# Performance work log

Measured on AMD Instinct MI355X. Metric: run time of the kernel, lower is better.

Reference implementation:

```python
import jax, jax.numpy as jnp
import numpy as np

TEMPERATURE = 0.07
NUM_UNIFY_CLASSES = 256


def setup_inputs() -> dict:
    key = jax.random.key(0)
    k1, k2, k3 = jax.random.split(key, 3)
    b, c, h, w = 16, 256, 128, 128
    # small-magnitude feats so exp(logits) stays finite at temperature 0.07
    feats = jax.random.normal(k1, (b, c, h, w), dtype=jnp.float32) * 0.05
    queue = jax.random.normal(k2, (NUM_UNIFY_CLASSES, c), dtype=jnp.float32)
    queue = queue / jnp.linalg.norm(queue, axis=1, keepdims=True)  # unit rows, as a memory bank would hold
    labels = jax.random.randint(k3, (b * h * w, NUM_UNIFY_CLASSES), 0, 2, dtype=jnp.int32)
    return {"feats": feats, "queue": queue, "labels": labels}


def reference(feats, queue, labels):
    b, c, h, w = feats.shape
    # [b,c,h,w] -> [N, c]
    f = jnp.transpose(feats, (0, 2, 3, 1)).reshape(-1, c)
    # [N, M] logits
    logits = (f @ queue.T) / TEMPERATURE
    pos_mask = labels.reshape(-1, NUM_UNIFY_CLASSES).astype(logits.dtype)
    neg_mask = 1.0 - pos_mask
    sum_neg = jnp.sum(jnp.exp(logits) * neg_mask, axis=1)   # [N]
    sum_pos = jnp.sum(jnp.exp(-logits) * pos_mask, axis=1)  # [N]
    loss = jnp.log(sum_neg * sum_pos + 1.0)                 # [N]
    lb_num = jnp.sum(loss != 0)
    return jnp.where(lb_num == 0, jnp.float32(0.0),
                     jnp.sum(loss) / jnp.maximum(lb_num, 1).astype(loss.dtype))
```

## Files before the change

kernel.cpp:

```cpp
#include <hip/hip_runtime.h>
#include <hip/hip_bf16.h>


typedef __bf16 bf16x8 __attribute__((ext_vector_type(8)));
typedef float floatx4 __attribute__((ext_vector_type(4)));

using gl_void = const __attribute__((address_space(1))) void;
using lds_void = __attribute__((address_space(3))) void;

union BFrag {
  unsigned int u32[4];
  bf16x8 bf;
};

__device__ __forceinline__ unsigned int pack_bf2(float a, float b) {
  unsigned int ua = __float_as_uint(a) + 0x8000u;
  unsigned int ub = __float_as_uint(b) + 0x8000u;
  return (ua >> 16) | (ub & 0xffff0000u);
}

__global__ void qprep(const float* __restrict__ queue,
                      unsigned short* __restrict__ qs,
                      float* __restrict__ accum) {
  const int gt = blockIdx.x * 256 + threadIdx.x;
  const int t = gt >> 6;
  const int lane = gt & 63;
  const int m = ((t >> 3) << 4) | (lane & 15);
  const int k0 = ((t & 7) << 5) | ((lane >> 4) << 3);
  const float* qr = queue + m * 256 + k0;
  const float TINV = 14.2857142857142857f;
  BFrag u;
#pragma unroll
  for (int j = 0; j < 4; ++j)
    u.u32[j] = pack_bf2(qr[2 * j] * TINV, qr[2 * j + 1] * TINV);
  *(uint4*)(qs + (size_t)gt * 8) = *(const uint4*)u.u32;
  if (gt == 0) { accum[0] = 0.0f; accum[1] = 0.0f; }
}

__global__ __launch_bounds__(256, 2) void pcl_main(
    const float* __restrict__ feats,
    const int* __restrict__ labels,
    const unsigned short* __restrict__ qs,
    float* __restrict__ accum) {
  __shared__ float Fl[16640];
  __shared__ float Red[8][64];

  const int bx = blockIdx.x;
  const int bidx = bx >> 8;
  const int hw0 = (bx & 255) << 6;
  const int tid = threadIdx.x;
  const int w = tid >> 6;
  const int lane = tid & 63;
  const int qd = lane >> 4;
  const int s = lane & 15;

  {
    const float* gbase = feats + (size_t)bidx * 256 * 16384 + hw0;
#pragma unroll
    for (int i = 0; i < 16; ++i) {
      const int g = (w << 4) + i;
      const float* gp = gbase + (size_t)((g << 2) + qd) * 16384 + (s << 2);
      float* lp = &Fl[g * 260];
      __builtin_amdgcn_global_load_lds((gl_void*)gp, (lds_void*)lp, 16, 0, 0);
    }
  }

  floatx4 acc[4][4];
#pragma unroll
  for (int mt = 0; mt < 4; ++mt)
#pragma unroll
    for (int nt = 0; nt < 4; ++nt)
      acc[mt][nt] = floatx4{0.0f, 0.0f, 0.0f, 0.0f};

  __syncthreads();

  const bf16x8* qfrag = (const bf16x8*)qs;
#pragma unroll
  for (int ks = 0; ks < 8; ++ks) {
    bf16x8 af[4];
#pragma unroll
    for (int mt = 0; mt < 4; ++mt) {
      const int t = ((((w << 2) + mt) << 3) | ks);
      af[mt] = qfrag[t * 64 + lane];
    }
    bf16x8 bfv[4];
#pragma unroll
    for (int nt = 0; nt < 4; ++nt) {
      const float* bp = &Fl[((ks << 3) + (qd << 1)) * 260 + (nt << 4) + s];
      BFrag u;
      u.u32[0] = pack_bf2(bp[0], bp[64]);
      u.u32[1] = pack_bf2(bp[128], bp[192]);
      u.u32[2] = pack_bf2(bp[260], bp[324]);
      u.u32[3] = pack_bf2(bp[388], bp[452]);
      bfv[nt] = u.bf;
    }
#pragma unroll
    for (int mt = 0; mt < 4; ++mt)
#pragma unroll
      for (int nt = 0; nt < 4; ++nt)
        acc[mt][nt] = __builtin_amdgcn_mfma_f32_16x16x32_bf16(af[mt], bfv[nt],
                                                              acc[mt][nt], 0, 0, 0);
  }

  const size_t nbase = (size_t)bx << 6;
  int4 lab[4][4];
#pragma unroll
  for (int mt = 0; mt < 4; ++mt)
#pragma unroll
    for (int nt = 0; nt < 4; ++nt)
      lab[mt][nt] = *(const int4*)(labels + ((nbase + (nt << 4) + s) << 8) +
                                   (w << 6) + (mt << 4) + (qd << 2));

  float nn[4] = {0.f, 0.f, 0.f, 0.f};
  float pp[4] = {0.f, 0.f, 0.f, 0.f};
#define ACCUM_TERM(LV, AV)                          \
  do {                                              \
    const float fl_ = (float)(LV);                  \
    const float l_ = (AV);                          \
    const float e_ = __expf(l_);                    \
    const float en_ = __expf(-l_);                  \
    nn[nt] += (1.0f - fl_) * e_;                    \
    pp[nt] += fl_ * en_;                            \
  } while (0)

#pragma unroll
  for (int mt = 0; mt < 4; ++mt) {
#pragma unroll
    for (int nt = 0; nt < 4; ++nt) {
      const int4 lb = lab[mt][nt];
      const floatx4 a = acc[mt][nt];
      ACCUM_TERM(lb.x, a[0]);
      ACCUM_TERM(lb.y, a[1]);
      ACCUM_TERM(lb.z, a[2]);
      ACCUM_TERM(lb.w, a[3]);
    }
  }
#undef ACCUM_TERM

#pragma unroll
  for (int nt = 0; nt < 4; ++nt) {
    nn[nt] += __shfl_xor(nn[nt], 16);
    nn[nt] += __shfl_xor(nn[nt], 32);
    pp[nt] += __shfl_xor(pp[nt], 16);
    pp[nt] += __shfl_xor(pp[nt], 32);
  }
  if (lane < 16) {
#pragma unroll
    for (int nt = 0; nt < 4; ++nt) {
      Red[(w << 1) | 0][(nt << 4) + lane] = nn[nt];
      Red[(w << 1) | 1][(nt << 4) + lane] = pp[nt];
    }
  }
  __syncthreads();

  if (tid < 64) {
    const float sn = Red[0][tid] + Red[2][tid] + Red[4][tid] + Red[6][tid];
    const float sp = Red[1][tid] + Red[3][tid] + Red[5][tid] + Red[7][tid];
    float loss = logf(sn * sp + 1.0f);
    float c = (loss != 0.0f) ? 1.0f : 0.0f;
#pragma unroll
    for (int off = 32; off > 0; off >>= 1) {
      loss += __shfl_xor(loss, off);
      c += __shfl_xor(c, off);
    }
    if (tid == 0) {
      atomicAdd(&accum[0], loss);
      atomicAdd(&accum[1], c);
    }
  }
}

__global__ void pcl_finalize(const float* __restrict__ accum,
                             float* __restrict__ out) {
  const float ssum = accum[0];
  const float c = accum[1];
  out[0] = (c != 0.0f) ? (ssum / c) : 0.0f;
}

extern "C" void kernel_launch(void* const* d_in, const int* in_sizes, int n_in,
                              void* d_out, int out_size, void* d_ws, size_t ws_size,
                              hipStream_t stream) {
  (void)in_sizes; (void)n_in; (void)out_size; (void)ws_size;
  const float* feats = (const float*)d_in[0];
  const float* queue = (const float*)d_in[1];
  const int* labels = (const int*)d_in[2];

  unsigned short* qs = (unsigned short*)d_ws;
  float* accum = (float*)((char*)d_ws + 256 * 256 * sizeof(unsigned short));

  qprep<<<32, 256, 0, stream>>>(queue, qs, accum);
  pcl_main<<<4096, 256, 0, stream>>>(feats, labels, qs, accum);
  pcl_finalize<<<1, 1, 0, stream>>>(accum, (float*)d_out);
}
```

Baseline: 534.5 us.

## Convert feats to bf16 once into LDS fragment layout and halve exp work

Each thread now loads feats straight into registers, packs them to bf16, and stores them to LDS already laid out as MFMA B fragments. The inner loop then reads each fragment with one 16-byte LDS load instead of eight scalar reads plus packing. LDS use drops from about 66KB to 32KB, and launch bounds rise to 4 blocks per CU to raise occupancy. Label loads are double-buffered across mt iterations, and the epilogue computes one exp per element chosen by the label instead of two. The risks are register pressure from the 64-float staging array under the tighter launch bound, and losing the asynchronous global-to-LDS copy.

After: 537.8 us. No clear change (+0.6%).

```diff
diff --git a/kernel.cpp b/kernel.cpp
--- a/kernel.cpp
+++ b/kernel.cpp
@@ -4,14 +4,6 @@
 
 typedef __bf16 bf16x8 __attribute__((ext_vector_type(8)));
 typedef float floatx4 __attribute__((ext_vector_type(4)));
-
-using gl_void = const __attribute__((address_space(1))) void;
-using lds_void = __attribute__((address_space(3))) void;
-
-union BFrag {
-  unsigned int u32[4];
-  bf16x8 bf;
-};
 
 __device__ __forceinline__ unsigned int pack_bf2(float a, float b) {
   unsigned int ua = __float_as_uint(a) + 0x8000u;
@@ -29,20 +21,20 @@
   const int k0 = ((t & 7) << 5) | ((lane >> 4) << 3);
   const float* qr = queue + m * 256 + k0;
   const float TINV = 14.2857142857142857f;
-  BFrag u;
+  union { unsigned int u32[4]; uint4 v; } u;
 #pragma unroll
   for (int j = 0; j < 4; ++j)
     u.u32[j] = pack_bf2(qr[2 * j] * TINV, qr[2 * j + 1] * TINV);
-  *(uint4*)(qs + (size_t)gt * 8) = *(const uint4*)u.u32;
+  *(uint4*)(qs + (size_t)gt * 8) = u.v;
   if (gt == 0) { accum[0] = 0.0f; accum[1] = 0.0f; }
 }
 
-__global__ __launch_bounds__(256, 2) void pcl_main(
+__global__ __launch_bounds__(256, 4) void pcl_main(
     const float* __restrict__ feats,
     const int* __restrict__ labels,
     const unsigned short* __restrict__ qs,
     float* __restrict__ accum) {
-  __shared__ float Fl[16640];
+  __shared__ uint4 Bs[2048];
   __shared__ float Red[8][64];
 
   const int bx = blockIdx.x;
@@ -54,15 +46,21 @@
   const int qd = lane >> 4;
   const int s = lane & 15;
 
-  {
-    const float* gbase = feats + (size_t)bidx * 256 * 16384 + hw0;
+  const float* gbase = feats + (size_t)bidx * 4194304 + (size_t)hw0;
+  float f[64];
 #pragma unroll
-    for (int i = 0; i < 16; ++i) {
-      const int g = (w << 4) + i;
-      const float* gp = gbase + (size_t)((g << 2) + qd) * 16384 + (s << 2);
-      float* lp = &Fl[g * 260];
-      __builtin_amdgcn_global_load_lds((gl_void*)gp, (lds_void*)lp, 16, 0, 0);
-    }
+  for (int i = 0; i < 64; ++i)
+    f[i] = gbase[(size_t)((w << 6) + i) * 16384 + lane];
+
+#pragma unroll
+  for (int g = 0; g < 8; ++g) {
+    uint4 u;
+    u.x = pack_bf2(f[8 * g + 0], f[8 * g + 1]);
+    u.y = pack_bf2(f[8 * g + 2], f[8 * g + 3]);
+    u.z = pack_bf2(f[8 * g + 4], f[8 * g + 5]);
+    u.w = pack_bf2(f[8 * g + 6], f[8 * g + 7]);
+    const int kg = (w << 3) + g;
+    Bs[(((kg >> 2) << 2) + qd) * 64 + ((kg & 3) << 4) + s] = u;
   }
 
   floatx4 acc[4][4];
@@ -75,25 +73,17 @@
   __syncthreads();
 
   const bf16x8* qfrag = (const bf16x8*)qs;
+  const bf16x8* Bf = (const bf16x8*)Bs;
 #pragma unroll
   for (int ks = 0; ks < 8; ++ks) {
     bf16x8 af[4];
 #pragma unroll
-    for (int mt = 0; mt < 4; ++mt) {
-      const int t = ((((w << 2) + mt) << 3) | ks);
-      af[mt] = qfrag[t * 64 + lane];
-    }
+    for (int mt = 0; mt < 4; ++mt)
+      af[mt] = qfrag[(((((w << 2) + mt) << 3) | ks) << 6) + lane];
     bf16x8 bfv[4];
 #pragma unroll
-    for (int nt = 0; nt < 4; ++nt) {
-      const float* bp = &Fl[((ks << 3) + (qd << 1)) * 260 + (nt << 4) + s];
-      BFrag u;
-      u.u32[0] = pack_bf2(bp[0], bp[64]);
-      u.u32[1] = pack_bf2(bp[128], bp[192]);
-      u.u32[2] = pack_bf2(bp[260], bp[324]);
-      u.u32[3] = pack_bf2(bp[388], bp[452]);
-      bfv[nt] = u.bf;
-    }
+    for (int nt = 0; nt < 4; ++nt)
+      bfv[nt] = Bf[(((ks << 2) + nt) << 6) + lane];
 #pragma unroll
     for (int mt = 0; mt < 4; ++mt)
 #pragma unroll
@@ -103,39 +93,46 @@
   }
 
   const size_t nbase = (size_t)bx << 6;
-  int4 lab[4][4];
-#pragma unroll
-  for (int mt = 0; mt < 4; ++mt)
-#pragma unroll
-    for (int nt = 0; nt < 4; ++nt)
-      lab[mt][nt] = *(const int4*)(labels + ((nbase + (nt << 4) + s) << 8) +
-                                   (w << 6) + (mt << 4) + (qd << 2));
+  const int cbase = (w << 6) | (qd << 2);
 
   float nn[4] = {0.f, 0.f, 0.f, 0.f};
   float pp[4] = {0.f, 0.f, 0.f, 0.f};
-#define ACCUM_TERM(LV, AV)                          \
-  do {                                              \
-    const float fl_ = (float)(LV);                  \
-    const float l_ = (AV);                          \
-    const float e_ = __expf(l_);                    \
-    const float en_ = __expf(-l_);                  \
-    nn[nt] += (1.0f - fl_) * e_;                    \
-    pp[nt] += fl_ * en_;                            \
+
+  int4 labA[4], labB[4];
+#pragma unroll
+  for (int nt = 0; nt < 4; ++nt)
+    labA[nt] = *(const int4*)(labels + ((nbase + (nt << 4) + s) << 8) + cbase);
+
+#define TERM(LV, AV, NTI)                                   \
+  do {                                                      \
+    const bool p_ = (LV) != 0;                              \
+    const float l_ = (AV);                                  \
+    const float e_ = __expf(p_ ? -l_ : l_);                 \
+    nn[NTI] += p_ ? 0.0f : e_;                              \
+    pp[NTI] += p_ ? e_ : 0.0f;                              \
   } while (0)
 
 #pragma unroll
   for (int mt = 0; mt < 4; ++mt) {
+    const int4* cur = (mt & 1) ? labB : labA;
+    int4* nxt = (mt & 1) ? labA : labB;
+    if (mt < 3) {
+#pragma unroll
+      for (int nt = 0; nt < 4; ++nt)
+        nxt[nt] = *(const int4*)(labels + ((nbase + (nt << 4) + s) << 8) +
+                                 cbase + ((mt + 1) << 4));
+    }
 #pragma unroll
     for (int nt = 0; nt < 4; ++nt) {
-      const int4 lb = lab[mt][nt];
+      const int4 lb = cur[nt];
       const floatx4 a = acc[mt][nt];
-      ACCUM_TERM(lb.x, a[0]);
-      ACCUM_TERM(lb.y, a[1]);
-      ACCUM_TERM(lb.z, a[2]);
-      ACCUM_TERM(lb.w, a[3]);
+      TERM(lb.x, a[0], nt);
+      TERM(lb.y, a[1], nt);
+      TERM(lb.z, a[2], nt);
+      TERM(lb.w, a[3], nt);
     }
   }
-#undef ACCUM_TERM
+#undef TERM
 
 #pragma unroll
   for (int nt = 0; nt < 4; ++nt) {
```
